# Kernel optimization log

Measured on AMD Instinct MI355X. Metric: run time of the kernel, lower is better.

The kernel has to match this reference:

```python
import jax, jax.numpy as jnp
import numpy as np

B, T, C = 2, 2048, 1024
NH = 16

def setup_inputs() -> dict:
    key = jax.random.key(0)
    ks = jax.random.split(key, 5)
    s = 0.02
    return {
        "x": jax.random.normal(ks[0], (B, T, C), dtype=jnp.float32),
        "w_attn": jax.random.normal(ks[1], (C, 3 * C), dtype=jnp.float32) * s,
        "b_attn": jax.random.normal(ks[2], (3 * C,), dtype=jnp.float32) * s,
        "w_proj": jax.random.normal(ks[3], (C, C), dtype=jnp.float32) * s,
        "b_proj": jax.random.normal(ks[4], (C,), dtype=jnp.float32) * s,
        "n_heads": NH,
    }

def reference(x, w_attn, b_attn, w_proj, b_proj, n_heads):
    Bx, Tx, Cx = x.shape
    hd = Cx // n_heads
    qkv = x @ w_attn + b_attn                      # [B,T,3C]
    q, k, v = jnp.split(qkv, 3, axis=-1)
    # [B,T,H,hd] -> [B,H,T,hd]
    q = q.reshape(Bx, Tx, n_heads, hd).transpose(0, 2, 1, 3)
    k = k.reshape(Bx, Tx, n_heads, hd).transpose(0, 2, 1, 3)
    v = v.reshape(Bx, Tx, n_heads, hd).transpose(0, 2, 1, 3)
    scale = 1.0 / np.sqrt(hd).astype(np.float32)
    att = jnp.einsum('bhqd,bhkd->bhqk', q, k) * scale   # [B,H,T,T]
    causal = jnp.tril(jnp.ones((Tx, Tx), dtype=bool))
    att = jnp.where(causal[None, None], att, -jnp.inf)
    att = jax.nn.softmax(att, axis=-1)
    y = jnp.einsum('bhqk,bhkd->bhqd', att, v)            # [B,H,T,hd]
    y = y.transpose(0, 2, 1, 3).reshape(Bx, Tx, Cx)
    return y @ w_proj + b_proj
```

## Files before the change

kernel.cpp:

```cpp
#include <hip/hip_runtime.h>

typedef __bf16 bf16x8 __attribute__((ext_vector_type(8)));
typedef float  f32x4  __attribute__((ext_vector_type(4)));

#define MFMA_BF16(a, b, c) __builtin_amdgcn_mfma_f32_16x16x32_bf16((a), (b), (c), 0, 0, 0)
#define NEG_INF (-1e30f)
#define SCL 0.18033688f

__device__ __forceinline__ void gld16(const void* g, void* l) {
  __builtin_amdgcn_global_load_lds(
      (const __attribute__((address_space(1))) void*)g,
      (__attribute__((address_space(3))) void*)l, 16, 0, 0);
}

__global__ void cast_f32_bf16(const float* __restrict__ in,
                              __bf16* __restrict__ out, int n) {
  int i = (blockIdx.x * 256 + threadIdx.x) * 8;
  if (i >= n) return;
  float4 a = *(const float4*)&in[i];
  float4 b = *(const float4*)&in[i + 4];
  bf16x8 v;
  v[0] = (__bf16)a.x; v[1] = (__bf16)a.y; v[2] = (__bf16)a.z; v[3] = (__bf16)a.w;
  v[4] = (__bf16)b.x; v[5] = (__bf16)b.y; v[6] = (__bf16)b.z; v[7] = (__bf16)b.w;
  *(bf16x8*)&out[i] = v;
}

__global__ void transpose_f32_bf16(const float* __restrict__ in,
                                   __bf16* __restrict__ out, int R, int C) {
  __shared__ float t[32][33];
  int tx = threadIdx.x & 31, ty = threadIdx.x >> 5;
  int x = blockIdx.x * 32 + tx;
  int y0 = blockIdx.y * 32 + ty;
#pragma unroll
  for (int i = 0; i < 4; ++i)
    t[ty + 8 * i][tx] = in[(size_t)(y0 + 8 * i) * C + x];
  __syncthreads();
  int x2 = blockIdx.y * 32 + tx;
#pragma unroll
  for (int i = 0; i < 4; ++i)
    out[(size_t)(blockIdx.x * 32 + ty + 8 * i) * R + x2] = (__bf16)t[tx][ty + 8 * i];
}

#define BN 128
#define BK 64

template <int BMT, typename TC>
__global__ __launch_bounds__(256) void gemm_bt_bias(
    const __bf16* __restrict__ A, const __bf16* __restrict__ Bt,
    const float* __restrict__ bias, TC* __restrict__ Cmat,
    int M, int N, int K) {
  constexpr int NI = BMT / 32;
  __shared__ __align__(16) __bf16 As[BMT * BK];
  __shared__ __align__(16) __bf16 Bs[BN * BK];
  int tid = threadIdx.x;
  int wave = tid >> 6, lane = tid & 63;
  int l16 = lane & 15, quad = lane >> 4;
  int wm = wave >> 1, wn = wave & 1;
  int m0 = blockIdx.y * BMT, n0 = blockIdx.x * BN;

  f32x4 acc[NI][4];
#pragma unroll
  for (int i = 0; i < NI; ++i)
#pragma unroll
    for (int j = 0; j < 4; ++j) acc[i][j] = (f32x4){0.f, 0.f, 0.f, 0.f};

  int row = tid >> 3;
  int kc = ((tid & 7) ^ ((tid >> 3) & 7)) * 8;
  int xr = (l16 & 7) * 8;

  for (int k0 = 0; k0 < K; k0 += BK) {
#pragma unroll
    for (int i = 0; i < NI; ++i)
      gld16(&A[(size_t)(m0 + row + i * 32) * K + k0 + kc],
            (char*)As + (i * 256 + wave * 64) * 16);
#pragma unroll
    for (int j = 0; j < 4; ++j)
      gld16(&Bt[(size_t)(n0 + row + j * 32) * K + k0 + kc],
            (char*)Bs + (j * 256 + wave * 64) * 16);
    __syncthreads();
#pragma unroll
    for (int ks = 0; ks < 2; ++ks) {
      bf16x8 af[NI], bfr[4];
#pragma unroll
      for (int i = 0; i < NI; ++i)
        af[i] = *(const bf16x8*)&As[(wm * (BMT / 2) + i * 16 + l16) * BK +
                                    ((ks * 32 + quad * 8) ^ xr)];
#pragma unroll
      for (int j = 0; j < 4; ++j)
        bfr[j] = *(const bf16x8*)&Bs[(wn * 64 + j * 16 + l16) * BK +
                                     ((ks * 32 + quad * 8) ^ xr)];
#pragma unroll
      for (int i = 0; i < NI; ++i)
#pragma unroll
        for (int j = 0; j < 4; ++j) acc[i][j] = MFMA_BF16(af[i], bfr[j], acc[i][j]);
    }
    __syncthreads();
  }
#pragma unroll
  for (int i = 0; i < NI; ++i) {
#pragma unroll
    for (int j = 0; j < 4; ++j) {
      int col = n0 + wn * 64 + j * 16 + l16;
      float bv = bias[col];
#pragma unroll
      for (int r = 0; r < 4; ++r) {
        int rw = m0 + wm * (BMT / 2) + i * 16 + quad * 4 + r;
        Cmat[(size_t)rw * N + col] = (TC)(acc[i][j][r] + bv);
      }
    }
  }
}

__global__ __launch_bounds__(256) void attn_causal(
    const __bf16* __restrict__ qkv, __bf16* __restrict__ y) {
  __shared__ __align__(16) __bf16 Kb[2][64 * 72];
  __shared__ __align__(16) __bf16 Vb[2][64 * 72];
  __shared__ __align__(16) __bf16 Ps[4][16 * 72];
  const int tid = threadIdx.x;
  const int wave = tid >> 6, lane = tid & 63;
  const int l16 = lane & 15, quad = lane >> 4;
  const int bh = blockIdx.x;
  const int b = bh >> 4, h = bh & 15;
  const int RS = 3072;
  const int key0 = tid >> 3;
  const int d0 = (tid & 7) * 8;
  const __bf16* kv0 = qkv + (size_t)(b * 2048) * RS + h * 64 + d0;

#pragma unroll 1
  for (int phase = 0; phase < 2; ++phase) {
    const int qt = phase ? (31 - (int)blockIdx.y) : (int)blockIdx.y;

    int qrow = b * 2048 + qt * 64 + wave * 16 + l16;
    const __bf16* qbase = qkv + (size_t)qrow * RS + h * 64;
    bf16x8 qf0 = *(const bf16x8*)(qbase + quad * 8);
    bf16x8 qf1 = *(const bf16x8*)(qbase + 32 + quad * 8);

    float l_i[4];
    f32x4 o[4];
#pragma unroll
    for (int r = 0; r < 4; ++r) l_i[r] = 0.f;
#pragma unroll
    for (int j = 0; j < 4; ++j) o[j] = (f32x4){0.f, 0.f, 0.f, 0.f};

    bf16x8 kreg[2], vreg[2];
#pragma unroll
    for (int i = 0; i < 2; ++i) {
      const __bf16* src = kv0 + (size_t)(key0 + 32 * i) * RS;
      kreg[i] = *(const bf16x8*)(src + 1024);
      vreg[i] = *(const bf16x8*)(src + 2048);
    }
#pragma unroll
    for (int i = 0; i < 2; ++i) {
      int key = key0 + 32 * i;
      *(bf16x8*)&Kb[0][key * 72 + d0] = kreg[i];
#pragma unroll
      for (int jj = 0; jj < 8; ++jj)
        Vb[0][(d0 + jj) * 72 + (key ^ d0)] = vreg[i][jj];
    }
    __syncthreads();

    for (int kt = 0; kt <= qt; ++kt) {
      const int cur = kt & 1;
      if (kt < qt) {
#pragma unroll
        for (int i = 0; i < 2; ++i) {
          const __bf16* src = kv0 + (size_t)((kt + 1) * 64 + key0 + 32 * i) * RS;
          kreg[i] = *(const bf16x8*)(src + 1024);
          vreg[i] = *(const bf16x8*)(src + 2048);
        }
      }

      f32x4 s[4];
#pragma unroll
      for (int j = 0; j < 4; ++j) s[j] = (f32x4){0.f, 0.f, 0.f, 0.f};
#pragma unroll
      for (int j = 0; j < 4; ++j) {
        bf16x8 kf0 = *(const bf16x8*)&Kb[cur][(j * 16 + l16) * 72 + quad * 8];
        bf16x8 kf1 = *(const bf16x8*)&Kb[cur][(j * 16 + l16) * 72 + 32 + quad * 8];
        s[j] = MFMA_BF16(qf0, kf0, s[j]);
        s[j] = MFMA_BF16(qf1, kf1, s[j]);
      }

      if (kt == qt) {
        int qg = wave * 16 + quad * 4;
#pragma unroll
        for (int j = 0; j < 4; ++j)
#pragma unroll
          for (int r = 0; r < 4; ++r)
            if (j * 16 + l16 > qg + r) s[j][r] = NEG_INF;
      }

#pragma unroll
      for (int r = 0; r < 4; ++r) {
#pragma unroll
        for (int j = 0; j < 4; ++j) {
          float p = __builtin_amdgcn_exp2f(s[j][r] * SCL);
          l_i[r] += p;
          Ps[wave][(quad * 4 + r) * 72 + j * 16 + l16] = (__bf16)p;
        }
      }

#pragma unroll
      for (int ks = 0; ks < 2; ++ks) {
        bf16x8 pf = *(const bf16x8*)&Ps[wave][l16 * 72 + ks * 32 + quad * 8];
#pragma unroll
        for (int j = 0; j < 4; ++j) {
          int dim = j * 16 + l16;
          bf16x8 vf = *(const bf16x8*)&Vb[cur][dim * 72 + ((ks * 32 + quad * 8) ^ (dim & 56))];
          o[j] = MFMA_BF16(pf, vf, o[j]);
        }
      }

      if (kt < qt) {
#pragma unroll
        for (int i = 0; i < 2; ++i) {
          int key = key0 + 32 * i;
          *(bf16x8*)&Kb[cur ^ 1][key * 72 + d0] = kreg[i];
#pragma unroll
          for (int jj = 0; jj < 8; ++jj)
            Vb[cur ^ 1][(d0 + jj) * 72 + (key ^ d0)] = vreg[i][jj];
        }
      }
      __syncthreads();
    }

    int orow = b * 2048 + qt * 64 + wave * 16 + quad * 4;
#pragma unroll
    for (int r = 0; r < 4; ++r) {
      float l = l_i[r];
      l += __shfl_xor(l, 1);
      l += __shfl_xor(l, 2);
      l += __shfl_xor(l, 4);
      l += __shfl_xor(l, 8);
      float inv = 1.f / l;
#pragma unroll
      for (int j = 0; j < 4; ++j)
        y[(size_t)(orow + r) * 1024 + h * 64 + j * 16 + l16] = (__bf16)(o[j][r] * inv);
    }
  }
}

extern "C" void kernel_launch(void* const* d_in, const int* in_sizes, int n_in,
                              void* d_out, int out_size, void* d_ws, size_t ws_size,
                              hipStream_t stream) {
  (void)in_sizes; (void)n_in; (void)out_size; (void)ws_size;
  const float* x      = (const float*)d_in[0];
  const float* w_attn = (const float*)d_in[1];
  const float* b_attn = (const float*)d_in[2];
  const float* w_proj = (const float*)d_in[3];
  const float* b_proj = (const float*)d_in[4];
  float* out = (float*)d_out;

  __bf16* wt_attn = (__bf16*)d_ws;
  __bf16* wt_proj = wt_attn + (size_t)3072 * 1024;
  __bf16* qkv     = wt_proj + (size_t)1024 * 1024;
  __bf16* ybuf    = qkv + (size_t)4096 * 3072;

  cast_f32_bf16<<<4096 * 1024 / 2048, 256, 0, stream>>>(x, ybuf, 4096 * 1024);

  transpose_f32_bf16<<<dim3(3072 / 32, 1024 / 32), 256, 0, stream>>>(w_attn, wt_attn, 1024, 3072);
  transpose_f32_bf16<<<dim3(1024 / 32, 1024 / 32), 256, 0, stream>>>(w_proj, wt_proj, 1024, 1024);

  gemm_bt_bias<128, __bf16><<<dim3(3072 / BN, 4096 / 128), 256, 0, stream>>>(
      ybuf, wt_attn, b_attn, qkv, 4096, 3072, 1024);

  attn_causal<<<dim3(2 * 16, 16), 256, 0, stream>>>(qkv, ybuf);

  gemm_bt_bias<64, float><<<dim3(1024 / BN, 4096 / 64), 256, 0, stream>>>(
      ybuf, wt_proj, b_proj, out, 4096, 1024, 1024);
}
```

Before: 186.9 us.

## Double attention query tile to 128 rows per block for K/V reuse

Each wave now processes two 16-row query sub-tiles (128 query rows per block instead of 64), so every K/V tile staged in shared memory feeds twice as many MFMAs. The grid's y dimension is halved and causal masking is applied to the last two key tiles with an offset. The aim is to halve K/V global loads and LDS staging per query row. In exchange, register pressure rises, the grid shrinks to 256 blocks, and the diagonal tiles do some wasted masked work.

```diff
diff --git a/kernel.cpp b/kernel.cpp
--- a/kernel.cpp
+++ b/kernel.cpp
@@ -115,7 +115,7 @@
     const __bf16* __restrict__ qkv, __bf16* __restrict__ y) {
   __shared__ __align__(16) __bf16 Kb[2][64 * 72];
   __shared__ __align__(16) __bf16 Vb[2][64 * 72];
-  __shared__ __align__(16) __bf16 Ps[4][16 * 72];
+  __shared__ __align__(16) __bf16 Ps[4][32 * 72];
   const int tid = threadIdx.x;
   const int wave = tid >> 6, lane = tid & 63;
   const int l16 = lane & 15, quad = lane >> 4;
@@ -128,19 +128,28 @@
 
 #pragma unroll 1
   for (int phase = 0; phase < 2; ++phase) {
-    const int qt = phase ? (31 - (int)blockIdx.y) : (int)blockIdx.y;
-
-    int qrow = b * 2048 + qt * 64 + wave * 16 + l16;
-    const __bf16* qbase = qkv + (size_t)qrow * RS + h * 64;
-    bf16x8 qf0 = *(const bf16x8*)(qbase + quad * 8);
-    bf16x8 qf1 = *(const bf16x8*)(qbase + 32 + quad * 8);
-
-    float l_i[4];
-    f32x4 o[4];
-#pragma unroll
-    for (int r = 0; r < 4; ++r) l_i[r] = 0.f;
-#pragma unroll
-    for (int j = 0; j < 4; ++j) o[j] = (f32x4){0.f, 0.f, 0.f, 0.f};
+    const int qt = phase ? (15 - (int)blockIdx.y) : (int)blockIdx.y;
+    const int KT = 2 * qt + 2;
+
+    bf16x8 qf[2][2];
+#pragma unroll
+    for (int t = 0; t < 2; ++t) {
+      int qrow = b * 2048 + qt * 128 + wave * 32 + t * 16 + l16;
+      const __bf16* qbase = qkv + (size_t)qrow * RS + h * 64;
+      qf[t][0] = *(const bf16x8*)(qbase + quad * 8);
+      qf[t][1] = *(const bf16x8*)(qbase + 32 + quad * 8);
+    }
+
+    float l_i[2][4];
+    f32x4 o[2][4];
+#pragma unroll
+    for (int t = 0; t < 2; ++t)
+#pragma unroll
+      for (int r = 0; r < 4; ++r) l_i[t][r] = 0.f;
+#pragma unroll
+    for (int t = 0; t < 2; ++t)
+#pragma unroll
+      for (int j = 0; j < 4; ++j) o[t][j] = (f32x4){0.f, 0.f, 0.f, 0.f};
 
     bf16x8 kreg[2], vreg[2];
 #pragma unroll
@@ -159,9 +168,9 @@
     }
     __syncthreads();
 
-    for (int kt = 0; kt <= qt; ++kt) {
+    for (int kt = 0; kt < KT; ++kt) {
       const int cur = kt & 1;
-      if (kt < qt) {
+      if (kt + 1 < KT) {
 #pragma unroll
         for (int i = 0; i < 2; ++i) {
           const __bf16* src = kv0 + (size_t)((kt + 1) * 64 + key0 + 32 * i) * RS;
@@ -170,48 +179,62 @@
         }
       }
 
-      f32x4 s[4];
-#pragma unroll
-      for (int j = 0; j < 4; ++j) s[j] = (f32x4){0.f, 0.f, 0.f, 0.f};
+      f32x4 s[2][4];
+#pragma unroll
+      for (int t = 0; t < 2; ++t)
+#pragma unroll
+        for (int j = 0; j < 4; ++j) s[t][j] = (f32x4){0.f, 0.f, 0.f, 0.f};
 #pragma unroll
       for (int j = 0; j < 4; ++j) {
         bf16x8 kf0 = *(const bf16x8*)&Kb[cur][(j * 16 + l16) * 72 + quad * 8];
         bf16x8 kf1 = *(const bf16x8*)&Kb[cur][(j * 16 + l16) * 72 + 32 + quad * 8];
-        s[j] = MFMA_BF16(qf0, kf0, s[j]);
-        s[j] = MFMA_BF16(qf1, kf1, s[j]);
-      }
-
-      if (kt == qt) {
-        int qg = wave * 16 + quad * 4;
-#pragma unroll
-        for (int j = 0; j < 4; ++j)
-#pragma unroll
-          for (int r = 0; r < 4; ++r)
-            if (j * 16 + l16 > qg + r) s[j][r] = NEG_INF;
-      }
-
-#pragma unroll
-      for (int r = 0; r < 4; ++r) {
-#pragma unroll
-        for (int j = 0; j < 4; ++j) {
-          float p = __builtin_amdgcn_exp2f(s[j][r] * SCL);
-          l_i[r] += p;
-          Ps[wave][(quad * 4 + r) * 72 + j * 16 + l16] = (__bf16)p;
-        }
-      }
+#pragma unroll
+        for (int t = 0; t < 2; ++t) {
+          s[t][j] = MFMA_BF16(qf[t][0], kf0, s[t][j]);
+          s[t][j] = MFMA_BF16(qf[t][1], kf1, s[t][j]);
+        }
+      }
+
+      if (kt >= 2 * qt) {
+        int off = (kt - 2 * qt) * 64;
+#pragma unroll
+        for (int t = 0; t < 2; ++t) {
+          int qg = wave * 32 + t * 16 + quad * 4;
+#pragma unroll
+          for (int j = 0; j < 4; ++j)
+#pragma unroll
+            for (int r = 0; r < 4; ++r)
+              if (j * 16 + l16 + off > qg + r) s[t][j][r] = NEG_INF;
+        }
+      }
+
+#pragma unroll
+      for (int t = 0; t < 2; ++t)
+#pragma unroll
+        for (int r = 0; r < 4; ++r)
+#pragma unroll
+          for (int j = 0; j < 4; ++j) {
+            float p = __builtin_amdgcn_exp2f(s[t][j][r] * SCL);
+            l_i[t][r] += p;
+            Ps[wave][(t * 16 + quad * 4 + r) * 72 + j * 16 + l16] = (__bf16)p;
+          }
 
 #pragma unroll
       for (int ks = 0; ks < 2; ++ks) {
-        bf16x8 pf = *(const bf16x8*)&Ps[wave][l16 * 72 + ks * 32 + quad * 8];
+        bf16x8 pf[2];
+#pragma unroll
+        for (int t = 0; t < 2; ++t)
+          pf[t] = *(const bf16x8*)&Ps[wave][(t * 16 + l16) * 72 + ks * 32 + quad * 8];
 #pragma unroll
         for (int j = 0; j < 4; ++j) {
           int dim = j * 16 + l16;
           bf16x8 vf = *(const bf16x8*)&Vb[cur][dim * 72 + ((ks * 32 + quad * 8) ^ (dim & 56))];
-          o[j] = MFMA_BF16(pf, vf, o[j]);
-        }
-      }
-
-      if (kt < qt) {
+#pragma unroll
+          for (int t = 0; t < 2; ++t) o[t][j] = MFMA_BF16(pf[t], vf, o[t][j]);
+        }
+      }
+
+      if (kt + 1 < KT) {
 #pragma unroll
         for (int i = 0; i < 2; ++i) {
           int key = key0 + 32 * i;
@@ -224,18 +247,21 @@
       __syncthreads();
     }
 
-    int orow = b * 2048 + qt * 64 + wave * 16 + quad * 4;
-#pragma unroll
-    for (int r = 0; r < 4; ++r) {
-      float l = l_i[r];
-      l += __shfl_xor(l, 1);
-      l += __shfl_xor(l, 2);
-      l += __shfl_xor(l, 4);
-      l += __shfl_xor(l, 8);
-      float inv = 1.f / l;
-#pragma unroll
-      for (int j = 0; j < 4; ++j)
-        y[(size_t)(orow + r) * 1024 + h * 64 + j * 16 + l16] = (__bf16)(o[j][r] * inv);
+#pragma unroll
+    for (int t = 0; t < 2; ++t) {
+      int orow = b * 2048 + qt * 128 + wave * 32 + t * 16 + quad * 4;
+#pragma unroll
+      for (int r = 0; r < 4; ++r) {
+        float l = l_i[t][r];
+        l += __shfl_xor(l, 1);
+        l += __shfl_xor(l, 2);
+        l += __shfl_xor(l, 4);
+        l += __shfl_xor(l, 8);
+        float inv = 1.f / l;
+#pragma unroll
+        for (int j = 0; j < 4; ++j)
+          y[(size_t)(orow + r) * 1024 + h * 64 + j * 16 + l16] = (__bf16)(o[t][j][r] * inv);
+      }
     }
   }
 }
@@ -264,7 +290,7 @@
   gemm_bt_bias<128, __bf16><<<dim3(3072 / BN, 4096 / 128), 256, 0, stream>>>(
       ybuf, wt_attn, b_attn, qkv, 4096, 3072, 1024);
 
-  attn_causal<<<dim3(2 * 16, 16), 256, 0, stream>>>(qkv, ybuf);
+  attn_causal<<<dim3(2 * 16, 8), 256, 0, stream>>>(qkv, ybuf);
 
   gemm_bt_bias<64, float><<<dim3(1024 / BN, 4096 / 64), 256, 0, stream>>>(
       ybuf, wt_proj, b_proj, out, 4096, 1024, 1024);
```

Result: slower. 203.7 us (+9.0%).

## Load K tiles directly into LDS and transpose score MFMA for vectorized P stores

Applied to the files above, without the earlier changes.

K tiles are now loaded with global_load_lds straight into an unpadded, XOR-swizzled shared buffer, removing the register staging and separate LDS writes for K. The QK^T MFMA operands are swapped so each lane holds four consecutive keys for a single query. This allows the probabilities to be written to shared memory as 4-element vectors and reduces the row-sum to one accumulator per lane, with a different shuffle pattern at the end. The cost is extra swizzle index arithmetic and reliance on correct async-load ordering with the existing barriers.

```diff
diff --git a/kernel.cpp b/kernel.cpp
--- a/kernel.cpp
+++ b/kernel.cpp
@@ -1,6 +1,7 @@
 #include <hip/hip_runtime.h>
 
 typedef __bf16 bf16x8 __attribute__((ext_vector_type(8)));
+typedef __bf16 bf16x4 __attribute__((ext_vector_type(4)));
 typedef float  f32x4  __attribute__((ext_vector_type(4)));
 
 #define MFMA_BF16(a, b, c) __builtin_amdgcn_mfma_f32_16x16x32_bf16((a), (b), (c), 0, 0, 0)
@@ -113,7 +114,7 @@
 
 __global__ __launch_bounds__(256) void attn_causal(
     const __bf16* __restrict__ qkv, __bf16* __restrict__ y) {
-  __shared__ __align__(16) __bf16 Kb[2][64 * 72];
+  __shared__ __align__(16) __bf16 Kb[2][64 * 64];
   __shared__ __align__(16) __bf16 Vb[2][64 * 72];
   __shared__ __align__(16) __bf16 Ps[4][16 * 72];
   const int tid = threadIdx.x;
@@ -122,9 +123,13 @@
   const int bh = blockIdx.x;
   const int b = bh >> 4, h = bh & 15;
   const int RS = 3072;
+
   const int key0 = tid >> 3;
   const int d0 = (tid & 7) * 8;
-  const __bf16* kv0 = qkv + (size_t)(b * 2048) * RS + h * 64 + d0;
+  const int kcs = ((tid & 7) ^ ((tid >> 3) & 7)) * 8;
+  const int xr = (l16 & 7) * 8;
+  const __bf16* kbase = qkv + (size_t)(b * 2048) * RS + 1024 + h * 64 + kcs;
+  const __bf16* vbase = qkv + (size_t)(b * 2048) * RS + 2048 + h * 64 + d0;
 
 #pragma unroll 1
   for (int phase = 0; phase < 2; ++phase) {
@@ -135,24 +140,21 @@
     bf16x8 qf0 = *(const bf16x8*)(qbase + quad * 8);
     bf16x8 qf1 = *(const bf16x8*)(qbase + 32 + quad * 8);
 
-    float l_i[4];
+    float l_i = 0.f;
     f32x4 o[4];
 #pragma unroll
-    for (int r = 0; r < 4; ++r) l_i[r] = 0.f;
-#pragma unroll
     for (int j = 0; j < 4; ++j) o[j] = (f32x4){0.f, 0.f, 0.f, 0.f};
 
-    bf16x8 kreg[2], vreg[2];
+    bf16x8 vreg[2];
 #pragma unroll
     for (int i = 0; i < 2; ++i) {
-      const __bf16* src = kv0 + (size_t)(key0 + 32 * i) * RS;
-      kreg[i] = *(const bf16x8*)(src + 1024);
-      vreg[i] = *(const bf16x8*)(src + 2048);
+      gld16(kbase + (size_t)(key0 + 32 * i) * RS,
+            (char*)Kb[0] + (i * 256 + tid) * 16);
+      vreg[i] = *(const bf16x8*)(vbase + (size_t)(key0 + 32 * i) * RS);
     }
 #pragma unroll
     for (int i = 0; i < 2; ++i) {
       int key = key0 + 32 * i;
-      *(bf16x8*)&Kb[0][key * 72 + d0] = kreg[i];
 #pragma unroll
       for (int jj = 0; jj < 8; ++jj)
         Vb[0][(d0 + jj) * 72 + (key ^ d0)] = vreg[i][jj];
@@ -164,9 +166,9 @@
       if (kt < qt) {
 #pragma unroll
         for (int i = 0; i < 2; ++i) {
-          const __bf16* src = kv0 + (size_t)((kt + 1) * 64 + key0 + 32 * i) * RS;
-          kreg[i] = *(const bf16x8*)(src + 1024);
-          vreg[i] = *(const bf16x8*)(src + 2048);
+          gld16(kbase + (size_t)((kt + 1) * 64 + key0 + 32 * i) * RS,
+                (char*)Kb[cur ^ 1] + (i * 256 + tid) * 16);
+          vreg[i] = *(const bf16x8*)(vbase + (size_t)((kt + 1) * 64 + key0 + 32 * i) * RS);
         }
       }
 
@@ -175,29 +177,31 @@
       for (int j = 0; j < 4; ++j) s[j] = (f32x4){0.f, 0.f, 0.f, 0.f};
 #pragma unroll
       for (int j = 0; j < 4; ++j) {
-        bf16x8 kf0 = *(const bf16x8*)&Kb[cur][(j * 16 + l16) * 72 + quad * 8];
-        bf16x8 kf1 = *(const bf16x8*)&Kb[cur][(j * 16 + l16) * 72 + 32 + quad * 8];
-        s[j] = MFMA_BF16(qf0, kf0, s[j]);
-        s[j] = MFMA_BF16(qf1, kf1, s[j]);
+        bf16x8 kf0 = *(const bf16x8*)&Kb[cur][(j * 16 + l16) * 64 + ((quad * 8) ^ xr)];
+        bf16x8 kf1 = *(const bf16x8*)&Kb[cur][(j * 16 + l16) * 64 + ((32 + quad * 8) ^ xr)];
+        s[j] = MFMA_BF16(kf0, qf0, s[j]);
+        s[j] = MFMA_BF16(kf1, qf1, s[j]);
       }
 
       if (kt == qt) {
-        int qg = wave * 16 + quad * 4;
+        int qg = wave * 16 + l16;
 #pragma unroll
         for (int j = 0; j < 4; ++j)
 #pragma unroll
           for (int r = 0; r < 4; ++r)
-            if (j * 16 + l16 > qg + r) s[j][r] = NEG_INF;
-      }
-
-#pragma unroll
-      for (int r = 0; r < 4; ++r) {
-#pragma unroll
-        for (int j = 0; j < 4; ++j) {
+            if (j * 16 + quad * 4 + r > qg) s[j][r] = NEG_INF;
+      }
+
+#pragma unroll
+      for (int j = 0; j < 4; ++j) {
+        bf16x4 pb;
+#pragma unroll
+        for (int r = 0; r < 4; ++r) {
           float p = __builtin_amdgcn_exp2f(s[j][r] * SCL);
-          l_i[r] += p;
-          Ps[wave][(quad * 4 + r) * 72 + j * 16 + l16] = (__bf16)p;
-        }
+          l_i += p;
+          pb[r] = (__bf16)p;
+        }
+        *(bf16x4*)&Ps[wave][l16 * 72 + j * 16 + quad * 4] = pb;
       }
 
 #pragma unroll
@@ -215,7 +219,6 @@
 #pragma unroll
         for (int i = 0; i < 2; ++i) {
           int key = key0 + 32 * i;
-          *(bf16x8*)&Kb[cur ^ 1][key * 72 + d0] = kreg[i];
 #pragma unroll
           for (int jj = 0; jj < 8; ++jj)
             Vb[cur ^ 1][(d0 + jj) * 72 + (key ^ d0)] = vreg[i][jj];
@@ -224,15 +227,13 @@
       __syncthreads();
     }
 
+    float lred = l_i;
+    lred += __shfl_xor(lred, 16);
+    lred += __shfl_xor(lred, 32);
     int orow = b * 2048 + qt * 64 + wave * 16 + quad * 4;
 #pragma unroll
     for (int r = 0; r < 4; ++r) {
-      float l = l_i[r];
-      l += __shfl_xor(l, 1);
-      l += __shfl_xor(l, 2);
-      l += __shfl_xor(l, 4);
-      l += __shfl_xor(l, 8);
-      float inv = 1.f / l;
+      float inv = 1.f / __shfl(lred, quad * 4 + r);
 #pragma unroll
       for (int j = 0; j < 4; ++j)
         y[(size_t)(orow + r) * 1024 + h * 64 + j * 16 + l16] = (__bf16)(o[j][r] * inv);
```

Measured after the change: 180.2 us. 1.04x faster.
